# Optimization experiments

Measured on AMD Instinct MI355X. Metric: run time of the kernel, lower is better.

Reference implementation:

```python
import jax, jax.numpy as jnp
import numpy as np

HIDDEN = 4096
N_HEADS = 32
N_KV_HEADS = 8
HEAD_DIM = 128
ROPE_THETA = 10000.0
LCK = 3          # number of suffix KV blocks
B = 2
S = 1024         # Q_LEN
VALID = 960      # valid_seq_len
NEG = -1e30


def rotate_half(x):
    h = x.shape[-1] // 2
    return jnp.concatenate([-x[..., h:], x[..., :h]], axis=-1)


def rope_cos_sin(seq_len, dim, theta, dtype):
    inv_freq = 1.0 / (theta ** (jnp.arange(0, dim, 2, dtype=jnp.float32) / dim))
    pos = jnp.arange(seq_len, dtype=jnp.float32)
    freqs = pos[:, None] * inv_freq[None, :]          # [S, dim/2]
    emb = jnp.concatenate([freqs, freqs], axis=-1)    # [S, dim]
    return jnp.cos(emb).astype(dtype), jnp.sin(emb).astype(dtype)


def setup_inputs() -> dict:
    key = jax.random.key(0)
    ks = jax.random.split(key, 8)
    w = 0.02
    return {
        "hidden_states": jax.random.normal(ks[0], (B, S, HIDDEN), jnp.float32),
        "k_suffix": jax.random.normal(ks[1], (B, N_KV_HEADS, LCK, S, HEAD_DIM), jnp.float32),
        "v_suffix": jax.random.normal(ks[2], (B, N_KV_HEADS, LCK, S, HEAD_DIM), jnp.float32),
        "Wq": jax.random.normal(ks[3], (HIDDEN, N_HEADS * HEAD_DIM), jnp.float32) * w,
        "Wk": jax.random.normal(ks[4], (HIDDEN, N_KV_HEADS * HEAD_DIM), jnp.float32) * w,
        "Wv": jax.random.normal(ks[5], (HIDDEN, N_KV_HEADS * HEAD_DIM), jnp.float32) * w,
        "Wo": jax.random.normal(ks[6], (N_HEADS * HEAD_DIM, HIDDEN), jnp.float32) * w,
        "valid_seq_len": VALID,
    }


def reference(hidden_states, k_suffix, v_suffix, Wq, Wk, Wv, Wo, valid_seq_len):
    b, s, _ = hidden_states.shape
    lck = k_suffix.shape[2]
    n_rep = N_HEADS // N_KV_HEADS
    scale = 1.0 / np.sqrt(HEAD_DIM)

    # projections: [B, H, S, D]
    q = (hidden_states @ Wq).reshape(b, s, N_HEADS, HEAD_DIM).transpose(0, 2, 1, 3)
    k0 = (hidden_states @ Wk).reshape(b, s, N_KV_HEADS, HEAD_DIM).transpose(0, 2, 1, 3)
    v0 = (hidden_states @ Wv).reshape(b, s, N_KV_HEADS, HEAD_DIM).transpose(0, 2, 1, 3)

    # RoPE on fresh q / k0
    cos, sin = rope_cos_sin(s, HEAD_DIM, ROPE_THETA, q.dtype)
    cos = cos[None, None]
    sin = sin[None, None]
    q = q * cos + rotate_half(q) * sin
    k0 = k0 * cos + rotate_half(k0) * sin

    # GQA expansion (repeat_kv)
    k0r = jnp.repeat(k0, n_rep, axis=1)                 # [B, H, S, D]
    v0r = jnp.repeat(v0, n_rep, axis=1)
    ks = jnp.repeat(k_suffix, n_rep, axis=1)            # [B, H, lck, S, D]
    vs = jnp.repeat(v_suffix, n_rep, axis=1)

    q_idx = jnp.arange(s)
    q_valid = q_idx < valid_seq_len                     # [S]

    # --- causal block (kv_idx < Q_LEN) ---
    sc_c = jnp.einsum('bhqd,bhkd->bhqk', q, k0r) * scale
    mask_c = (q_idx[:, None] >= q_idx[None, :]) & q_valid[None, :] & q_valid[:, None]
    sc_c = jnp.where(mask_c[None, None], sc_c, NEG)

    # --- suffix blocks: only diagonal kv_idx = q_idx + j*Q_LEN survives ---
    # score for suffix block j at query q is q . k_suffix[j, q]
    sc_s = jnp.einsum('bhqd,bhjqd->bhqj', q, ks) * scale    # [B, H, S, lck]
    # diag kv_mod == q_idx, so suffix valid iff q_idx < valid_seq_len
    sc_s = jnp.where(q_valid[None, None, :, None], sc_s, NEG)

    logits = jnp.concatenate([sc_c, sc_s], axis=-1)      # [B, H, S, S+lck]
    probs = jax.nn.softmax(logits, axis=-1)

    out = jnp.einsum('bhqk,bhkd->bhqd', probs[..., :s], v0r) + \
          jnp.einsum('bhqj,bhjqd->bhqd', probs[..., s:], vs)
    # fully-masked rows (q >= valid_seq_len) output zero like flash attention
    out = out * q_valid[None, None, :, None].astype(out.dtype)

    out = out.transpose(0, 2, 1, 3).reshape(b, s, N_HEADS * HEAD_DIM)
    return out @ Wo


if __name__ == "__main__":
    o = reference(**setup_inputs())
    print(o.shape, o.dtype)
```

## Files before the change

### kernel.cpp

```cpp
#include <hip/hip_runtime.h>

#define HIDDEN 4096
#define NH 32
#define NKV 8
#define HD 128
#define LCK 3
#define BB 2
#define SS 1024
#define MTOT (BB * SS)

typedef unsigned short u16;
typedef __attribute__((ext_vector_type(8))) short s16x8;
typedef __attribute__((ext_vector_type(4))) float f32x4;

__device__ __forceinline__ u16 f2bf(float f) {
  unsigned u = __builtin_bit_cast(unsigned, f);
  u += 0x7fffu + ((u >> 16) & 1u);
  return (u16)(u >> 16);
}
__device__ __forceinline__ float bf2f(u16 h) {
  return __builtin_bit_cast(float, (unsigned)h << 16);
}
__device__ __forceinline__ void gld16(const void* g, void* l) {
  __builtin_amdgcn_global_load_lds((const __attribute__((address_space(1))) void*)g,
                                   (__attribute__((address_space(3))) void*)l, 16, 0, 0);
}

__global__ __launch_bounds__(256) void convert_h(const float* __restrict__ in,
                                                 u16* __restrict__ out, int n4) {
  int i = blockIdx.x * 256 + threadIdx.x;
  if (i >= n4) return;
  float4 v = ((const float4*)in)[i];
  uint2 o;
  o.x = (unsigned)f2bf(v.x) | ((unsigned)f2bf(v.y) << 16);
  o.y = (unsigned)f2bf(v.z) | ((unsigned)f2bf(v.w) << 16);
  ((uint2*)out)[i] = o;
}

__global__ __launch_bounds__(256) void transpose_w(const float* __restrict__ W,
                                                   u16* __restrict__ Wt, int K, int N) {
  __shared__ float tile[64][65];
  const int n0 = blockIdx.x * 64, k0 = blockIdx.y * 64;
  const int ty = threadIdx.x >> 6, tx = threadIdx.x & 63;
#pragma unroll
  for (int i = 0; i < 16; ++i) {
    int r = ty * 16 + i;
    tile[r][tx] = W[(size_t)(k0 + r) * N + n0 + tx];
  }
  __syncthreads();
#pragma unroll
  for (int i = 0; i < 16; ++i) {
    int r = ty * 16 + i;
    Wt[(size_t)(n0 + r) * K + k0 + tx] = f2bf(tile[tx][r]);
  }
}

template <bool BF16OUT>
__global__ __launch_bounds__(512, 2) void gemm_bt(
    const u16* __restrict__ A, const u16* __restrict__ Bt,
    void* C0v, void* C1v, void* C2v, int N, int K, int n1, int n2) {
  __shared__ __align__(16) char smem[131072];
  const int tid = threadIdx.x, lane = tid & 63, w = tid >> 6;
  const int wr = w >> 2, wc = w & 3;
  const int col16 = lane & 15, quad = lane >> 4;

  const int nbx = gridDim.x;
  const int nwg = nbx * gridDim.y;
  int fid = blockIdx.y * nbx + blockIdx.x;
  {
    const int q = nwg >> 3, r = nwg & 7;
    const int xcd = fid & 7, lid = fid >> 3;
    fid = (xcd < r ? xcd * (q + 1) : r * (q + 1) + (xcd - r) * q) + lid;
  }
  const int bm = (fid / nbx) << 8, bn = (fid % nbx) << 8;

  const int rowlane = lane >> 2;
  const int collane = ((lane & 3) * 8) ^ ((lane & 32) ? 16 : 0);
  const u16* aSrc = A + (size_t)(bm + ((w >> 1) << 4) + rowlane) * K + ((w & 1) << 5) + collane;
  const u16* bSrc = Bt + (size_t)(bn + ((w >> 1) << 4) + rowlane) * K + ((w & 1) << 5) + collane;
  const int laneoff = (lane & 15) * 64 + (((lane >> 4) << 4) ^ ((lane & 8) << 2));
  const int NT = K >> 6;

#define STG(opOfs, src, buf, h, tt)                                              \
  do {                                                                           \
    gld16((src) + (size_t)((h) * 128) * K + (size_t)(tt) * 64,                   \
          smem + (buf) * 65536 + (opOfs) +                                       \
              ((((h) * 8 + (w >> 1)) * 2 + (w & 1)) << 10));                     \
    gld16((src) + (size_t)((h) * 128 + 64) * K + (size_t)(tt) * 64,              \
          smem + (buf) * 65536 + (opOfs) +                                       \
              ((((h) * 8 + 4 + (w >> 1)) * 2 + (w & 1)) << 10));                 \
  } while (0)
#define BARX asm volatile("s_barrier" ::: "memory")
#define LGK0                                                                     \
  do {                                                                           \
    asm volatile("s_waitcnt lgkmcnt(0)" ::: "memory");                           \
    __builtin_amdgcn_sched_barrier(0);                                           \
  } while (0)

  f32x4 acc[8][4];
#pragma unroll
  for (int f = 0; f < 8; ++f)
#pragma unroll
    for (int g = 0; g < 4; ++g) acc[f][g] = (f32x4){0.f, 0.f, 0.f, 0.f};

  STG(32768, bSrc, 0, 0, 0);
  STG(32768, bSrc, 0, 1, 0);
  STG(0, aSrc, 0, 0, 0);
  STG(0, aSrc, 0, 1, 0);
  STG(32768, bSrc, 1, 0, 1);
  STG(32768, bSrc, 1, 1, 1);
  STG(0, aSrc, 1, 0, 1);
  asm volatile("s_waitcnt vmcnt(6)" ::: "memory");
  BARX;

  for (int kt = 0; kt < NT; ++kt) {
    const int buf = kt & 1;
    const char* Af = smem + buf * 65536 + wr * 16384 + laneoff;
    const char* Bf = smem + buf * 65536 + 32768 + wc * 8192 + laneoff;
    s16x8 b0[4], b1[4], a0[4], a1[4];
#pragma unroll
    for (int g = 0; g < 4; ++g) {
      b0[g] = *(const s16x8*)(Bf + (g * 2 + 0) * 1024);
      b1[g] = *(const s16x8*)(Bf + (g * 2 + 1) * 1024);
    }
#pragma unroll
    for (int f = 0; f < 4; ++f) a0[f] = *(const s16x8*)(Af + (f * 2 + 0) * 1024);
    if (kt + 1 < NT) STG(0, aSrc, (kt + 1) & 1, 1, kt + 1);
    BARX; LGK0;
    __builtin_amdgcn_s_setprio(1);
#pragma unroll
    for (int f = 0; f < 4; ++f)
#pragma unroll
      for (int g = 0; g < 4; ++g)
        acc[f][g] = __builtin_amdgcn_mfma_f32_16x16x32_bf16(a0[f], b0[g], acc[f][g], 0, 0, 0);
    __builtin_amdgcn_s_setprio(0);
    BARX;
#pragma unroll
    for (int f = 0; f < 4; ++f) a1[f] = *(const s16x8*)(Af + ((4 + f) * 2 + 0) * 1024);
#pragma unroll
    for (int f = 0; f < 4; ++f) a0[f] = *(const s16x8*)(Af + (f * 2 + 1) * 1024);
    if (kt + 2 < NT) STG(32768, bSrc, buf, 0, kt + 2);
    BARX; LGK0;
    __builtin_amdgcn_s_setprio(1);
#pragma unroll
    for (int f = 0; f < 4; ++f)
#pragma unroll
      for (int g = 0; g < 4; ++g)
        acc[4 + f][g] = __builtin_amdgcn_mfma_f32_16x16x32_bf16(a1[f], b0[g], acc[4 + f][g], 0, 0, 0);
    __builtin_amdgcn_s_setprio(0);
    BARX;
#pragma unroll
    for (int f = 0; f < 4; ++f) a1[f] = *(const s16x8*)(Af + ((4 + f) * 2 + 1) * 1024);
    if (kt + 2 < NT) STG(32768, bSrc, buf, 1, kt + 2);
    BARX; LGK0;
    __builtin_amdgcn_s_setprio(1);
#pragma unroll
    for (int f = 0; f < 4; ++f)
#pragma unroll
      for (int g = 0; g < 4; ++g)
        acc[f][g] = __builtin_amdgcn_mfma_f32_16x16x32_bf16(a0[f], b1[g], acc[f][g], 0, 0, 0);
    __builtin_amdgcn_s_setprio(0);
    BARX;
    if (kt + 2 < NT) STG(0, aSrc, buf, 0, kt + 2);
    BARX; LGK0;
    __builtin_amdgcn_s_setprio(1);
#pragma unroll
    for (int f = 0; f < 4; ++f)
#pragma unroll
      for (int g = 0; g < 4; ++g)
        acc[4 + f][g] = __builtin_amdgcn_mfma_f32_16x16x32_bf16(a1[f], b1[g], acc[4 + f][g], 0, 0, 0);
    __builtin_amdgcn_s_setprio(0);
    if (kt < NT - 2) asm volatile("s_waitcnt vmcnt(6)" ::: "memory");
    else if (kt == NT - 2) asm volatile("s_waitcnt vmcnt(0)" ::: "memory");
    BARX;
  }
#undef STG
#undef BARX
#undef LGK0

  float* Cf; u16* Ch; int ldc, nb;
  if (bn < n1)      { ldc = n1;      nb = bn;      Cf = (float*)C0v; Ch = (u16*)C0v; }
  else if (bn < n2) { ldc = n2 - n1; nb = bn - n1; Cf = (float*)C1v; Ch = (u16*)C1v; }
  else              { ldc = N - n2;  nb = bn - n2; Cf = (float*)C2v; Ch = (u16*)C2v; }
#pragma unroll
  for (int f = 0; f < 8; ++f)
#pragma unroll
    for (int g = 0; g < 4; ++g)
#pragma unroll
      for (int r = 0; r < 4; ++r) {
        size_t off = (size_t)(bm + wr * 128 + f * 16 + quad * 4 + r) * ldc +
                     nb + wc * 64 + g * 16 + col16;
        if (BF16OUT) Ch[off] = f2bf(acc[f][g][r]);
        else         Cf[off] = acc[f][g][r];
      }
}

__global__ __launch_bounds__(256) void rope_convert(const u16* __restrict__ Qin,
                                                    const u16* __restrict__ Kin,
                                                    u16* __restrict__ Qout,
                                                    u16* __restrict__ Kout) {
  const int per_row = (NH + NKV) * 64;
  int idx = blockIdx.x * 256 + threadIdx.x;
  if (idx >= MTOT * per_row) return;
  int row = idx / per_row;
  int rem = idx - row * per_row;
  int hh = rem >> 6, i = rem & 63;
  int s = row & (SS - 1), b = row >> 10;

  float invf = __expf((float)i * (-9.210340371976184f / 64.0f));
  float ang = (float)s * invf;
  float cv = cosf(ang), sv = sinf(ang);

  if (hh < NH) {
    const u16* src = Qin + (size_t)row * (NH * HD) + hh * HD;
    u16* dst = Qout + (((size_t)(b * NH + hh)) * SS + s) * HD;
    float x0 = bf2f(src[i]), x1 = bf2f(src[i + 64]);
    dst[i] = f2bf(x0 * cv - x1 * sv);
    dst[i + 64] = f2bf(x1 * cv + x0 * sv);
  } else {
    int kh = hh - NH;
    const u16* src = Kin + (size_t)row * (NKV * HD) + kh * HD;
    u16* dst = Kout + (((size_t)(b * NKV + kh)) * SS + s) * HD;
    float x0 = bf2f(src[i]), x1 = bf2f(src[i + 64]);
    dst[i] = f2bf(x0 * cv - x1 * sv);
    dst[i + 64] = f2bf(x1 * cv + x0 * sv);
  }
}

__global__ __launch_bounds__(256) void transpose_v(const u16* __restrict__ V0,
                                                   u16* __restrict__ Vt) {
  __shared__ u16 tile[64][65];
  const int s0 = blockIdx.x * 64, d0 = blockIdx.y * 64;
  const int bk = blockIdx.z;
  const int b = bk >> 3, kvh = bk & 7;
  const int ty = threadIdx.x >> 6, tx = threadIdx.x & 63;
#pragma unroll
  for (int i = 0; i < 16; ++i) {
    int r = ty * 16 + i;
    tile[r][tx] = V0[((size_t)(b * SS + s0 + r)) * (NKV * HD) + kvh * HD + d0 + tx];
  }
  __syncthreads();
#pragma unroll
  for (int i = 0; i < 16; ++i) {
    int r = ty * 16 + i;
    Vt[((size_t)bk * HD + d0 + r) * SS + s0 + tx] = tile[tx][r];
  }
}

__global__ __launch_bounds__(256) void attn_mfma(
    const u16* __restrict__ Qbf, const u16* __restrict__ Kbf, const u16* __restrict__ Vt,
    const float* __restrict__ ksuf, const float* __restrict__ vsuf,
    u16* __restrict__ AObf, const int* __restrict__ validp) {
  __shared__ u16 Ksh[16][32][8];
  __shared__ u16 Vsh[4][128][8];
  __shared__ u16 Psh[4][4][16][8];

  const int qt = 63 - (int)blockIdx.x;
  const int q0 = qt * 16;
  const int kvh = blockIdx.y, b = blockIdx.z;
  const int t = threadIdx.x, lane = t & 63, w = t >> 6;
  const int col = lane & 15, quad = lane >> 4;
  const int h = (kvh << 2) + w;
  const int valid = *validp;

  size_t obase = ((size_t)(b * SS + q0 + quad * 4)) * (NH * HD) + h * HD + col;
  if (q0 >= valid) {
#pragma unroll
    for (int r = 0; r < 4; ++r) {
      size_t o = obase + (size_t)r * (NH * HD);
#pragma unroll
      for (int nt = 0; nt < 8; ++nt) AObf[o + 16 * nt] = 0;
    }
    return;
  }

  const float scale = 0.08838834764831845f;
  const u16* qptr = Qbf + (((size_t)(b * NH + h)) * SS + q0 + col) * HD;
  s16x8 qf[4];
#pragma unroll
  for (int ds = 0; ds < 4; ++ds) qf[ds] = *(const s16x8*)(qptr + ds * 32 + quad * 8);

  const u16* kbase = Kbf + ((size_t)(b * NKV + kvh)) * SS * HD;
  const u16* vbase = Vt + ((size_t)(b * NKV + kvh)) * HD * SS;

  float m_[4], l_[4];
  f32x4 O_[8];
#pragma unroll
  for (int r = 0; r < 4; ++r) { m_[r] = -1e30f; l_[r] = 0.f; }
#pragma unroll
  for (int nt = 0; nt < 8; ++nt) O_[nt] = (f32x4){0.f, 0.f, 0.f, 0.f};

  const int ntiles = (q0 + 47) >> 5;
  const int o0 = w * 1024 + lane * 16;
  const int o1 = o0 + 4096;

  for (int ti = 0; ti < ntiles; ++ti) {
    const int k0 = ti * 32;
    {
      int dc = o0 >> 9, kr = (o0 >> 4) & 31;
      gld16(kbase + (size_t)(k0 + kr) * HD + dc * 8, (char*)Ksh + w * 1024);
      dc = o1 >> 9; kr = (o1 >> 4) & 31;
      gld16(kbase + (size_t)(k0 + kr) * HD + dc * 8, (char*)Ksh + w * 1024 + 4096);
      int kc = o0 >> 11, d = (o0 >> 4) & 127;
      gld16(vbase + (size_t)d * SS + k0 + kc * 8, (char*)Vsh + w * 1024);
      kc = o1 >> 11; d = (o1 >> 4) & 127;
      gld16(vbase + (size_t)d * SS + k0 + kc * 8, (char*)Vsh + w * 1024 + 4096);
    }
    __syncthreads();

    f32x4 S0 = (f32x4){0.f,0.f,0.f,0.f}, S1 = (f32x4){0.f,0.f,0.f,0.f};
#pragma unroll
    for (int ds = 0; ds < 4; ++ds) {
      s16x8 kf0 = *(const s16x8*)&Ksh[ds * 4 + quad][col][0];
      s16x8 kf1 = *(const s16x8*)&Ksh[ds * 4 + quad][col + 16][0];
      S0 = __builtin_amdgcn_mfma_f32_16x16x32_bf16(qf[ds], kf0, S0, 0, 0, 0);
      S1 = __builtin_amdgcn_mfma_f32_16x16x32_bf16(qf[ds], kf1, S1, 0, 0, 0);
    }

    float al[4], p0v[4], p1v[4];
#pragma unroll
    for (int r = 0; r < 4; ++r) {
      int row_g = q0 + quad * 4 + r;
      float s0 = (k0 + col > row_g) ? -1e30f : S0[r] * scale;
      float s1 = (k0 + 16 + col > row_g) ? -1e30f : S1[r] * scale;
      float tm = fmaxf(s0, s1);
      tm = fmaxf(tm, __shfl_xor(tm, 1));
      tm = fmaxf(tm, __shfl_xor(tm, 2));
      tm = fmaxf(tm, __shfl_xor(tm, 4));
      tm = fmaxf(tm, __shfl_xor(tm, 8));
      float mn = fmaxf(m_[r], tm);
      float a = __expf(m_[r] - mn);
      float p0 = __expf(s0 - mn), p1 = __expf(s1 - mn);
      float rs = p0 + p1;
      rs += __shfl_xor(rs, 1);
      rs += __shfl_xor(rs, 2);
      rs += __shfl_xor(rs, 4);
      rs += __shfl_xor(rs, 8);
      l_[r] = l_[r] * a + rs;
      m_[r] = mn;
      al[r] = a; p0v[r] = p0; p1v[r] = p1;
    }
#pragma unroll
    for (int nt = 0; nt < 8; ++nt)
#pragma unroll
      for (int r = 0; r < 4; ++r) O_[nt][r] *= al[r];

    {
      int kcA = col >> 3, kk = col & 7;
#pragma unroll
      for (int r = 0; r < 4; ++r) {
        Psh[w][kcA][quad * 4 + r][kk] = f2bf(p0v[r]);
        Psh[w][2 + kcA][quad * 4 + r][kk] = f2bf(p1v[r]);
      }
    }
    __syncthreads();

    s16x8 pf = *(const s16x8*)&Psh[w][quad][col][0];
#pragma unroll
    for (int nt = 0; nt < 8; ++nt) {
      s16x8 vf = *(const s16x8*)&Vsh[quad][col + 16 * nt][0];
      O_[nt] = __builtin_amdgcn_mfma_f32_16x16x32_bf16(pf, vf, O_[nt], 0, 0, 0);
    }
    __syncthreads();
  }

  float sr[3][4];
#pragma unroll
  for (int j = 0; j < 3; ++j) {
    const float* krow = ksuf + ((((size_t)(b * NKV + kvh) * LCK + j)) * SS + q0 + col) * HD;
    float p = 0.f;
#pragma unroll
    for (int ds = 0; ds < 4; ++ds) {
      const float* kp = krow + ds * 32 + quad * 8;
#pragma unroll
      for (int e = 0; e < 8; ++e) p += bf2f((u16)qf[ds][e]) * kp[e];
    }
    p += __shfl_xor(p, 16);
    p += __shfl_xor(p, 32);
    p *= scale;
#pragma unroll
    for (int r = 0; r < 4; ++r) sr[j][r] = __shfl(p, quad * 4 + r);
  }
#pragma unroll
  for (int r = 0; r < 4; ++r) {
    int q = q0 + quad * 4 + r;
    float ms = fmaxf(fmaxf(sr[0][r], sr[1][r]), sr[2][r]);
    float mn = fmaxf(m_[r], ms);
    float a = __expf(m_[r] - mn);
    float p0 = __expf(sr[0][r] - mn);
    float p1 = __expf(sr[1][r] - mn);
    float p2 = __expf(sr[2][r] - mn);
    l_[r] = l_[r] * a + p0 + p1 + p2;
    const float* v0r = vsuf + ((((size_t)(b * NKV + kvh) * LCK + 0)) * SS + q) * HD + col;
    const float* v1r = v0r + (size_t)SS * HD;
    const float* v2r = v1r + (size_t)SS * HD;
#pragma unroll
    for (int nt = 0; nt < 8; ++nt)
      O_[nt][r] = O_[nt][r] * a + p0 * v0r[16 * nt] + p1 * v1r[16 * nt] + p2 * v2r[16 * nt];
    m_[r] = mn;
  }

#pragma unroll
  for (int r = 0; r < 4; ++r) {
    int q = q0 + quad * 4 + r;
    size_t o = obase + (size_t)r * (NH * HD);
    if (q >= valid) {
#pragma unroll
      for (int nt = 0; nt < 8; ++nt) AObf[o + 16 * nt] = 0;
    } else {
      float inv = 1.f / l_[r];
#pragma unroll
      for (int nt = 0; nt < 8; ++nt) AObf[o + 16 * nt] = f2bf(O_[nt][r] * inv);
    }
  }
}

extern "C" void kernel_launch(void* const* d_in, const int* in_sizes, int n_in,
                              void* d_out, int out_size, void* d_ws, size_t ws_size,
                              hipStream_t stream) {
  const float* hidden = (const float*)d_in[0];
  const float* ksuf = (const float*)d_in[1];
  const float* vsuf = (const float*)d_in[2];
  const float* Wq = (const float*)d_in[3];
  const float* Wk = (const float*)d_in[4];
  const float* Wv = (const float*)d_in[5];
  const float* Wo = (const float*)d_in[6];
  const int* validp = (const int*)d_in[7];
  float* out = (float*)d_out;

  char* W = (char*)d_ws;
  u16* Hbf  = (u16*)(W + 0);
  u16* WqT  = (u16*)(W + ((size_t)16 << 20));
  u16* WkT  = (u16*)(W + ((size_t)48 << 20));
  u16* WvT  = (u16*)(W + ((size_t)56 << 20));
  u16* Qbf0 = (u16*)(W + ((size_t)64 << 20));
  u16* K0bf = (u16*)(W + ((size_t)80 << 20));
  u16* V0bf = (u16*)(W + ((size_t)84 << 20));
  u16* Kbf  = (u16*)(W + ((size_t)88 << 20));
  u16* Vt   = (u16*)(W + ((size_t)92 << 20));
  u16* Qbf  = (u16*)(W + 0);
  u16* WoT  = (u16*)(W + ((size_t)16 << 20));
  u16* AObf = (u16*)(W + ((size_t)64 << 20));

  convert_h<<<(MTOT * HIDDEN / 4 + 255) / 256, 256, 0, stream>>>(hidden, Hbf, MTOT * HIDDEN / 4);
  transpose_w<<<dim3(64, 64), 256, 0, stream>>>(Wq, WqT, HIDDEN, NH * HD);
  transpose_w<<<dim3(16, 64), 256, 0, stream>>>(Wk, WkT, HIDDEN, NKV * HD);
  transpose_w<<<dim3(16, 64), 256, 0, stream>>>(Wv, WvT, HIDDEN, NKV * HD);
  gemm_bt<true><<<dim3(24, 8), 512, 0, stream>>>(
      Hbf, WqT, Qbf0, K0bf, V0bf, 6144, HIDDEN, 4096, 5120);
  transpose_w<<<dim3(64, 64), 256, 0, stream>>>(Wo, WoT, NH * HD, HIDDEN);
  rope_convert<<<(MTOT * (NH + NKV) * 64 + 255) / 256, 256, 0, stream>>>(Qbf0, K0bf, Qbf, Kbf);
  transpose_v<<<dim3(16, 2, BB * NKV), 256, 0, stream>>>(V0bf, Vt);
  attn_mfma<<<dim3(64, NKV, BB), 256, 0, stream>>>(Qbf, Kbf, Vt, ksuf, vsuf, AObf, validp);
  gemm_bt<false><<<dim3(16, 8), 512, 0, stream>>>(
      AObf, WoT, out, out, out, HIDDEN, NH * HD, 4096, 4096);
}
```

Measured before the change: 618.1 us.

## Rewrite attention kernel to compute transposed scores and drop shared-memory staging

The attention kernel now computes S^T = K·Q^T with MFMA, so each lane owns one query row. The softmax reduction becomes two cross-quad shuffles instead of four per row. K and V fragments are read straight from global memory rather than staged in LDS, which removes all __syncthreads and LDS traffic, and KV tiles grow from 32 to 64. The PV step uses half-zero-padded 16x16x32 MFMAs (only 4 of 8 k-slots used), which wastes matrix throughput and doubles the MFMA count. The 1D grid is remapped so heavy q-tiles for all heads launch first, and output and suffix-V accesses are vectorised.

```diff
diff --git a/kernel.cpp b/kernel.cpp
--- a/kernel.cpp
+++ b/kernel.cpp
@@ -11,6 +11,7 @@
 
 typedef unsigned short u16;
 typedef __attribute__((ext_vector_type(8))) short s16x8;
+typedef __attribute__((ext_vector_type(4))) short s16x4;
 typedef __attribute__((ext_vector_type(4))) float f32x4;
 
 __device__ __forceinline__ u16 f2bf(float f) {
@@ -251,31 +252,27 @@
     const u16* __restrict__ Qbf, const u16* __restrict__ Kbf, const u16* __restrict__ Vt,
     const float* __restrict__ ksuf, const float* __restrict__ vsuf,
     u16* __restrict__ AObf, const int* __restrict__ validp) {
-  __shared__ u16 Ksh[16][32][8];
-  __shared__ u16 Vsh[4][128][8];
-  __shared__ u16 Psh[4][4][16][8];
-
-  const int qt = 63 - (int)blockIdx.x;
+  const int bid = (int)blockIdx.x;
+  const int qt = 63 - (bid >> 4);
+  const int kvh = bid & 7, b = (bid >> 3) & 1;
   const int q0 = qt * 16;
-  const int kvh = blockIdx.y, b = blockIdx.z;
-  const int t = threadIdx.x, lane = t & 63, w = t >> 6;
+  const int lane = threadIdx.x & 63, w = threadIdx.x >> 6;
   const int col = lane & 15, quad = lane >> 4;
   const int h = (kvh << 2) + w;
   const int valid = *validp;
-
-  size_t obase = ((size_t)(b * SS + q0 + quad * 4)) * (NH * HD) + h * HD + col;
+  const int q = q0 + col;
+
+  size_t orow = ((size_t)(b * SS + q)) * (NH * HD) + h * HD;
   if (q0 >= valid) {
-#pragma unroll
-    for (int r = 0; r < 4; ++r) {
-      size_t o = obase + (size_t)r * (NH * HD);
-#pragma unroll
-      for (int nt = 0; nt < 8; ++nt) AObf[o + 16 * nt] = 0;
-    }
+    ushort4 z = {0, 0, 0, 0};
+#pragma unroll
+    for (int nt = 0; nt < 8; ++nt)
+      *(ushort4*)(AObf + orow + 16 * nt + quad * 4) = z;
     return;
   }
 
   const float scale = 0.08838834764831845f;
-  const u16* qptr = Qbf + (((size_t)(b * NH + h)) * SS + q0 + col) * HD;
+  const u16* qptr = Qbf + (((size_t)(b * NH + h)) * SS + q) * HD;
   s16x8 qf[4];
 #pragma unroll
   for (int ds = 0; ds < 4; ++ds) qf[ds] = *(const s16x8*)(qptr + ds * 32 + quad * 8);
@@ -283,134 +280,129 @@
   const u16* kbase = Kbf + ((size_t)(b * NKV + kvh)) * SS * HD;
   const u16* vbase = Vt + ((size_t)(b * NKV + kvh)) * HD * SS;
 
-  float m_[4], l_[4];
+  float m_ = -1e30f, l_ = 0.f;
   f32x4 O_[8];
 #pragma unroll
-  for (int r = 0; r < 4; ++r) { m_[r] = -1e30f; l_[r] = 0.f; }
-#pragma unroll
   for (int nt = 0; nt < 8; ++nt) O_[nt] = (f32x4){0.f, 0.f, 0.f, 0.f};
 
-  const int ntiles = (q0 + 47) >> 5;
-  const int o0 = w * 1024 + lane * 16;
-  const int o1 = o0 + 4096;
+  const int ntiles = (q0 + 16 + 63) >> 6;
 
   for (int ti = 0; ti < ntiles; ++ti) {
-    const int k0 = ti * 32;
-    {
-      int dc = o0 >> 9, kr = (o0 >> 4) & 31;
-      gld16(kbase + (size_t)(k0 + kr) * HD + dc * 8, (char*)Ksh + w * 1024);
-      dc = o1 >> 9; kr = (o1 >> 4) & 31;
-      gld16(kbase + (size_t)(k0 + kr) * HD + dc * 8, (char*)Ksh + w * 1024 + 4096);
-      int kc = o0 >> 11, d = (o0 >> 4) & 127;
-      gld16(vbase + (size_t)d * SS + k0 + kc * 8, (char*)Vsh + w * 1024);
-      kc = o1 >> 11; d = (o1 >> 4) & 127;
-      gld16(vbase + (size_t)d * SS + k0 + kc * 8, (char*)Vsh + w * 1024 + 4096);
-    }
-    __syncthreads();
-
-    f32x4 S0 = (f32x4){0.f,0.f,0.f,0.f}, S1 = (f32x4){0.f,0.f,0.f,0.f};
-#pragma unroll
-    for (int ds = 0; ds < 4; ++ds) {
-      s16x8 kf0 = *(const s16x8*)&Ksh[ds * 4 + quad][col][0];
-      s16x8 kf1 = *(const s16x8*)&Ksh[ds * 4 + quad][col + 16][0];
-      S0 = __builtin_amdgcn_mfma_f32_16x16x32_bf16(qf[ds], kf0, S0, 0, 0, 0);
-      S1 = __builtin_amdgcn_mfma_f32_16x16x32_bf16(qf[ds], kf1, S1, 0, 0, 0);
-    }
-
-    float al[4], p0v[4], p1v[4];
-#pragma unroll
-    for (int r = 0; r < 4; ++r) {
-      int row_g = q0 + quad * 4 + r;
-      float s0 = (k0 + col > row_g) ? -1e30f : S0[r] * scale;
-      float s1 = (k0 + 16 + col > row_g) ? -1e30f : S1[r] * scale;
-      float tm = fmaxf(s0, s1);
-      tm = fmaxf(tm, __shfl_xor(tm, 1));
-      tm = fmaxf(tm, __shfl_xor(tm, 2));
-      tm = fmaxf(tm, __shfl_xor(tm, 4));
-      tm = fmaxf(tm, __shfl_xor(tm, 8));
-      float mn = fmaxf(m_[r], tm);
-      float a = __expf(m_[r] - mn);
-      float p0 = __expf(s0 - mn), p1 = __expf(s1 - mn);
-      float rs = p0 + p1;
-      rs += __shfl_xor(rs, 1);
-      rs += __shfl_xor(rs, 2);
-      rs += __shfl_xor(rs, 4);
-      rs += __shfl_xor(rs, 8);
-      l_[r] = l_[r] * a + rs;
-      m_[r] = mn;
-      al[r] = a; p0v[r] = p0; p1v[r] = p1;
-    }
+    const int k0 = ti * 64;
+    f32x4 S[4];
+#pragma unroll
+    for (int ks = 0; ks < 4; ++ks) {
+      const u16* kp = kbase + (size_t)(k0 + ks * 16 + col) * HD + quad * 8;
+      f32x4 s = (f32x4){0.f, 0.f, 0.f, 0.f};
+#pragma unroll
+      for (int ds = 0; ds < 4; ++ds) {
+        s16x8 kf = *(const s16x8*)(kp + ds * 32);
+        s = __builtin_amdgcn_mfma_f32_16x16x32_bf16(kf, qf[ds], s, 0, 0, 0);
+      }
+      S[ks] = s;
+    }
+    float sc[16];
+    float tm = -1e30f;
+#pragma unroll
+    for (int ks = 0; ks < 4; ++ks)
+#pragma unroll
+      for (int r = 0; r < 4; ++r) {
+        int kg = k0 + ks * 16 + quad * 4 + r;
+        float v = (kg > q) ? -1e30f : S[ks][r] * scale;
+        sc[ks * 4 + r] = v;
+        tm = fmaxf(tm, v);
+      }
+    tm = fmaxf(tm, __shfl_xor(tm, 16));
+    tm = fmaxf(tm, __shfl_xor(tm, 32));
+    float mn = fmaxf(m_, tm);
+    float a = __expf(m_ - mn);
+    float pv[16];
+    float rs = 0.f;
+#pragma unroll
+    for (int i = 0; i < 16; ++i) {
+      pv[i] = __expf(sc[i] - mn);
+      rs += pv[i];
+    }
+    rs += __shfl_xor(rs, 16);
+    rs += __shfl_xor(rs, 32);
+    l_ = l_ * a + rs;
+    m_ = mn;
 #pragma unroll
     for (int nt = 0; nt < 8; ++nt)
 #pragma unroll
-      for (int r = 0; r < 4; ++r) O_[nt][r] *= al[r];
-
-    {
-      int kcA = col >> 3, kk = col & 7;
-#pragma unroll
-      for (int r = 0; r < 4; ++r) {
-        Psh[w][kcA][quad * 4 + r][kk] = f2bf(p0v[r]);
-        Psh[w][2 + kcA][quad * 4 + r][kk] = f2bf(p1v[r]);
+      for (int r = 0; r < 4; ++r) O_[nt][r] *= a;
+
+#pragma unroll
+    for (int ks = 0; ks < 4; ++ks) {
+      s16x8 pb;
+      pb[0] = (short)f2bf(pv[ks * 4 + 0]);
+      pb[1] = (short)f2bf(pv[ks * 4 + 1]);
+      pb[2] = (short)f2bf(pv[ks * 4 + 2]);
+      pb[3] = (short)f2bf(pv[ks * 4 + 3]);
+      pb[4] = 0; pb[5] = 0; pb[6] = 0; pb[7] = 0;
+      const u16* vp0 = vbase + (size_t)col * SS + k0 + ks * 16 + quad * 4;
+#pragma unroll
+      for (int nt = 0; nt < 8; ++nt) {
+        s16x4 vv = *(const s16x4*)(vp0 + (size_t)(16 * nt) * SS);
+        s16x8 av;
+        av[0] = vv[0]; av[1] = vv[1]; av[2] = vv[2]; av[3] = vv[3];
+        av[4] = 0; av[5] = 0; av[6] = 0; av[7] = 0;
+        O_[nt] = __builtin_amdgcn_mfma_f32_16x16x32_bf16(av, pb, O_[nt], 0, 0, 0);
       }
     }
-    __syncthreads();
-
-    s16x8 pf = *(const s16x8*)&Psh[w][quad][col][0];
-#pragma unroll
-    for (int nt = 0; nt < 8; ++nt) {
-      s16x8 vf = *(const s16x8*)&Vsh[quad][col + 16 * nt][0];
-      O_[nt] = __builtin_amdgcn_mfma_f32_16x16x32_bf16(pf, vf, O_[nt], 0, 0, 0);
-    }
-    __syncthreads();
-  }
-
-  float sr[3][4];
+  }
+
+  float sp[3];
 #pragma unroll
   for (int j = 0; j < 3; ++j) {
-    const float* krow = ksuf + ((((size_t)(b * NKV + kvh) * LCK + j)) * SS + q0 + col) * HD;
+    const float* kr = ksuf + ((((size_t)(b * NKV + kvh) * LCK + j)) * SS + q) * HD + quad * 8;
     float p = 0.f;
 #pragma unroll
-    for (int ds = 0; ds < 4; ++ds) {
-      const float* kp = krow + ds * 32 + quad * 8;
-#pragma unroll
-      for (int e = 0; e < 8; ++e) p += bf2f((u16)qf[ds][e]) * kp[e];
-    }
+    for (int ds = 0; ds < 4; ++ds)
+#pragma unroll
+      for (int e = 0; e < 8; ++e) p += bf2f((u16)qf[ds][e]) * kr[ds * 32 + e];
     p += __shfl_xor(p, 16);
     p += __shfl_xor(p, 32);
-    p *= scale;
-#pragma unroll
-    for (int r = 0; r < 4; ++r) sr[j][r] = __shfl(p, quad * 4 + r);
-  }
-#pragma unroll
-  for (int r = 0; r < 4; ++r) {
-    int q = q0 + quad * 4 + r;
-    float ms = fmaxf(fmaxf(sr[0][r], sr[1][r]), sr[2][r]);
-    float mn = fmaxf(m_[r], ms);
-    float a = __expf(m_[r] - mn);
-    float p0 = __expf(sr[0][r] - mn);
-    float p1 = __expf(sr[1][r] - mn);
-    float p2 = __expf(sr[2][r] - mn);
-    l_[r] = l_[r] * a + p0 + p1 + p2;
-    const float* v0r = vsuf + ((((size_t)(b * NKV + kvh) * LCK + 0)) * SS + q) * HD + col;
+    sp[j] = p * scale;
+  }
+  {
+    float ms = fmaxf(fmaxf(sp[0], sp[1]), sp[2]);
+    float mn = fmaxf(m_, ms);
+    float a = __expf(m_ - mn);
+    float e0 = __expf(sp[0] - mn);
+    float e1 = __expf(sp[1] - mn);
+    float e2 = __expf(sp[2] - mn);
+    l_ = l_ * a + e0 + e1 + e2;
+    const float* v0r = vsuf + ((((size_t)(b * NKV + kvh) * LCK + 0)) * SS + q) * HD + quad * 4;
     const float* v1r = v0r + (size_t)SS * HD;
     const float* v2r = v1r + (size_t)SS * HD;
 #pragma unroll
+    for (int nt = 0; nt < 8; ++nt) {
+      float4 x0 = *(const float4*)(v0r + 16 * nt);
+      float4 x1 = *(const float4*)(v1r + 16 * nt);
+      float4 x2 = *(const float4*)(v2r + 16 * nt);
+      O_[nt][0] = O_[nt][0] * a + e0 * x0.x + e1 * x1.x + e2 * x2.x;
+      O_[nt][1] = O_[nt][1] * a + e0 * x0.y + e1 * x1.y + e2 * x2.y;
+      O_[nt][2] = O_[nt][2] * a + e0 * x0.z + e1 * x1.z + e2 * x2.z;
+      O_[nt][3] = O_[nt][3] * a + e0 * x0.w + e1 * x1.w + e2 * x2.w;
+    }
+  }
+
+  if (q >= valid) {
+    ushort4 z = {0, 0, 0, 0};
+#pragma unroll
     for (int nt = 0; nt < 8; ++nt)
-      O_[nt][r] = O_[nt][r] * a + p0 * v0r[16 * nt] + p1 * v1r[16 * nt] + p2 * v2r[16 * nt];
-    m_[r] = mn;
-  }
-
-#pragma unroll
-  for (int r = 0; r < 4; ++r) {
-    int q = q0 + quad * 4 + r;
-    size_t o = obase + (size_t)r * (NH * HD);
-    if (q >= valid) {
-#pragma unroll
-      for (int nt = 0; nt < 8; ++nt) AObf[o + 16 * nt] = 0;
-    } else {
-      float inv = 1.f / l_[r];
-#pragma unroll
-      for (int nt = 0; nt < 8; ++nt) AObf[o + 16 * nt] = f2bf(O_[nt][r] * inv);
+      *(ushort4*)(AObf + orow + 16 * nt + quad * 4) = z;
+  } else {
+    float inv = 1.f / l_;
+#pragma unroll
+    for (int nt = 0; nt < 8; ++nt) {
+      ushort4 o;
+      o.x = f2bf(O_[nt][0] * inv);
+      o.y = f2bf(O_[nt][1] * inv);
+      o.z = f2bf(O_[nt][2] * inv);
+      o.w = f2bf(O_[nt][3] * inv);
+      *(ushort4*)(AObf + orow + 16 * nt + quad * 4) = o;
     }
   }
 }
@@ -451,7 +443,7 @@
   transpose_w<<<dim3(64, 64), 256, 0, stream>>>(Wo, WoT, NH * HD, HIDDEN);
   rope_convert<<<(MTOT * (NH + NKV) * 64 + 255) / 256, 256, 0, stream>>>(Qbf0, K0bf, Qbf, Kbf);
   transpose_v<<<dim3(16, 2, BB * NKV), 256, 0, stream>>>(V0bf, Vt);
-  attn_mfma<<<dim3(64, NKV, BB), 256, 0, stream>>>(Qbf, Kbf, Vt, ksuf, vsuf, AObf, validp);
+  attn_mfma<<<dim3(1024), 256, 0, stream>>>(Qbf, Kbf, Vt, ksuf, vsuf, AObf, validp);
   gemm_bt<false><<<dim3(16, 8), 512, 0, stream>>>(
       AObf, WoT, out, out, out, HIDDEN, NH * HD, 4096, 4096);
 }
```

After: 673.7 us. 9.0% more time.
